# Performance work log

Measured on AMD Instinct MI355X. Metric: run time of the kernel, lower is better.

The kernel has to match this reference:

```python
import jax, jax.numpy as jnp
import numpy as np
from jax import lax

B, T, L = 16, 200, 250
IDIM, ODIM, DUNITS = 512, 80, 1024
ATT_DIM, ACONV_CHANS, ACONV_K = 128, 32, 31
PRENET = 256


def setup_inputs() -> dict:
    key = jax.random.key(0)
    ks = iter(jax.random.split(key, 40))
    def nrm(shape, fan_in):
        return jax.random.normal(next(ks), shape, jnp.float32) * (fan_in ** -0.5)
    inp = {}
    inp['hs'] = jax.random.normal(next(ks), (B, T, IDIM), jnp.float32)
    inp['hlens'] = jax.random.randint(next(ks), (B,), T // 2, T + 1)
    inp['ys'] = jax.random.normal(next(ks), (B, L, ODIM), jnp.float32)
    # location-aware attention params
    inp['W_enc'] = nrm((IDIM, ATT_DIM), IDIM)
    inp['b_enc'] = jnp.zeros((ATT_DIM,), jnp.float32)
    inp['W_dec'] = nrm((DUNITS, ATT_DIM), DUNITS)
    inp['W_att'] = nrm((ACONV_CHANS, ATT_DIM), ACONV_CHANS)
    inp['loc_conv_w'] = nrm((ACONV_CHANS, 1, ACONV_K), ACONV_K)
    inp['gvec_w'] = nrm((ATT_DIM,), ATT_DIM)
    inp['gvec_b'] = jnp.zeros((), jnp.float32)
    # prenet (no bias, dropout off in eval)
    inp['prenet_W1'] = nrm((ODIM, PRENET), ODIM)
    inp['prenet_W2'] = nrm((PRENET, PRENET), PRENET)
    # LSTM cells (torch gate order i,f,g,o; bih+bhh folded into one bias)
    in0 = IDIM + PRENET
    inp['Wih0'] = nrm((4 * DUNITS, in0), in0)
    inp['Whh0'] = nrm((4 * DUNITS, DUNITS), DUNITS)
    inp['b0'] = jnp.zeros((4 * DUNITS,), jnp.float32)
    inp['Wih1'] = nrm((4 * DUNITS, DUNITS), DUNITS)
    inp['Whh1'] = nrm((4 * DUNITS, DUNITS), DUNITS)
    inp['b1'] = jnp.zeros((4 * DUNITS,), jnp.float32)
    # output heads
    inp['feat_W'] = nrm((DUNITS, ODIM), DUNITS)
    inp['prob_W'] = nrm((DUNITS,), DUNITS)
    inp['prob_b'] = jnp.zeros((), jnp.float32)
    # postnet: conv(no bias) + BN(eval; running mean=0, var=1 folded away) + tanh
    inp['post_w_in'] = nrm((512, ODIM, 5), 5 * ODIM)
    inp['post_g_in'] = jnp.ones((512,), jnp.float32)
    inp['post_b_in'] = jnp.zeros((512,), jnp.float32)
    inp['post_w_mid'] = nrm((3, 512, 512, 5), 5 * 512)
    inp['post_g_mid'] = jnp.ones((3, 512), jnp.float32)
    inp['post_b_mid'] = jnp.zeros((3, 512), jnp.float32)
    inp['post_w_out'] = nrm((ODIM, 512, 5), 5 * 512)
    inp['post_g_out'] = jnp.ones((ODIM,), jnp.float32)
    inp['post_b_out'] = jnp.zeros((ODIM,), jnp.float32)
    return inp


def _conv1d(x, w, pad):
    # x: [B, Cin, T], w: [Cout, Cin, K]
    return lax.conv_general_dilated(x, w, (1,), [(pad, pad)],
                                    dimension_numbers=('NCH', 'OIH', 'NCH'))


def _lstm(x, h, c, Wih, Whh, b):
    g = x @ Wih.T + h @ Whh.T + b
    i, f, gg, o = jnp.split(g, 4, axis=-1)
    c2 = jax.nn.sigmoid(f) * c + jax.nn.sigmoid(i) * jnp.tanh(gg)
    return jax.nn.sigmoid(o) * jnp.tanh(c2), c2


def reference(hs, hlens, ys, W_enc, b_enc, W_dec, W_att, loc_conv_w, gvec_w, gvec_b,
              prenet_W1, prenet_W2, Wih0, Whh0, b0, Wih1, Whh1, b1,
              feat_W, prob_W, prob_b,
              post_w_in, post_g_in, post_b_in, post_w_mid, post_g_mid, post_b_mid,
              post_w_out, post_g_out, post_b_out):
    mask = jnp.arange(T)[None, :] < hlens[:, None]            # [B,T]
    pre_enc = hs @ W_enc + b_enc                              # [B,T,A] precomputed
    # teacher forcing: prenet input at step i is ys[:, i-1] (zeros at i=0);
    # prenet has no recurrent dependency -> vectorize over time
    prev = jnp.concatenate([jnp.zeros((B, 1, ODIM), hs.dtype), ys[:, :L - 1]], axis=1)
    pren = jax.nn.relu(jax.nn.relu(prev @ prenet_W1) @ prenet_W2)  # [B,L,256]
    att_w0 = mask.astype(hs.dtype) / hlens[:, None].astype(hs.dtype)
    z = jnp.zeros((B, DUNITS), hs.dtype)
    carry0 = (z, z, z, z, att_w0)

    def step(carry, pren_t):
        z0, c0, z1, c1, att_w = carry
        conv = _conv1d(att_w[:, None, :], loc_conv_w, ACONV_K // 2)   # [B,C,T]
        e = jnp.tanh(pre_enc + jnp.einsum('bct,ca->bta', conv, W_att)
                     + (z0 @ W_dec)[:, None, :]) @ gvec_w + gvec_b    # [B,T]
        e = jnp.where(mask, e, -1e30)
        w = jax.nn.softmax(2.0 * e, axis=1)                           # scaling=2.0
        att_c = jnp.einsum('bt,btd->bd', w, hs)
        x = jnp.concatenate([att_c, pren_t], axis=1)
        z0n, c0n = _lstm(x, z0, c0, Wih0, Whh0, b0)
        z1n, c1n = _lstm(z0n, z1, c1, Wih1, Whh1, b1)
        return (z0n, c0n, z1n, c1n, w), (z1n @ feat_W, z1n @ prob_W + prob_b)

    _, (outs, probs) = lax.scan(step, carry0, jnp.swapaxes(pren, 0, 1))
    outs = jnp.transpose(outs, (1, 2, 0))   # [B, odim, L] (matches torch.stack dim=2)
    probs = probs.T                         # [B, L]
    # postnet (BN in eval with running mean=0/var=1 reduces to gamma*x+beta)
    h = jnp.tanh(post_g_in[:, None] * _conv1d(outs, post_w_in, 2) + post_b_in[:, None])
    for i in range(3):
        h = jnp.tanh(post_g_mid[i][:, None] * _conv1d(h, post_w_mid[i], 2)
                     + post_b_mid[i][:, None])
    h = post_g_out[:, None] * _conv1d(h, post_w_out, 2) + post_b_out[:, None]
    post_outs = outs + h
    return jnp.swapaxes(post_outs, 1, 2), jnp.swapaxes(outs, 1, 2), probs
```

## Files before the change

### kernel.cpp

```cpp
#include <hip/hip_runtime.h>
#include <cstdint>
#include <cstddef>

constexpr int B_ = 16, T_ = 200, L_ = 250;
constexpr int IDIM = 512, ODIM = 80, DUNITS = 1024;
constexpr int ADIM = 128, ACH = 32, AK = 31;
constexpr int PRE = 256;
constexpr int TPAD = 208;

typedef _Float16 h16;
typedef _Float16 half8 __attribute__((ext_vector_type(8)));
typedef _Float16 half4 __attribute__((ext_vector_type(4)));
typedef float f32x4 __attribute__((ext_vector_type(4)));

constexpr int FSTEP = 352;
constexpr int FZ0W = 0, FZ0AGG = 256, FDPW = 288, FAW = 320;

constexpr size_t OFF_PE    = 0;
constexpr size_t OFF_H0H   = 851968;
constexpr size_t OFF_Z1H   = 917504;
constexpr size_t OFF_ATTC  = 983040;
constexpr size_t OFF_DP    = 999424;
constexpr size_t OFF_FLAGS = 1007616;
constexpr size_t ZERO_BYTES= 1359616;
constexpr size_t OFF_MB    = 1359616;
constexpr size_t OFF_WDR   = 1367808;
constexpr size_t OFF_PREN  = 1629952;
constexpr size_t OFF_HSH   = 3677952;
constexpr size_t OFF_W0AH  = 6954752;
constexpr size_t OFF_WHH0  = 13246208;
constexpr size_t OFF_WI1   = 21634816;
constexpr size_t OFF_WHH1  = 30023424;
constexpr size_t OFF_Z1ALL = 38412032;
constexpr size_t OFF_OUTS  = 54796032;
constexpr size_t OFF_PA    = 56076032;
constexpr size_t OFF_PB    = 64268032;

__device__ __forceinline__ float fsig(float x) {
  x = fminf(fmaxf(x, -30.f), 30.f);
  return __builtin_amdgcn_rcpf(1.f + __expf(-x));
}
__device__ __forceinline__ float ftanh(float x) {
  x = fminf(fmaxf(x, -15.f), 15.f);
  const float e = __expf(2.f * x);
  return (e - 1.f) * __builtin_amdgcn_rcpf(e + 1.f);
}
__device__ __forceinline__ f32x4 mfma16(half8 a, half8 b, f32x4 c) {
  return __builtin_amdgcn_mfma_f32_16x16x32_f16(a, b, c, 0, 0, 0);
}
__device__ __forceinline__ half8 load8_agent(const h16* p) {
  union { unsigned long long q[2]; half8 v; } cv;
  cv.q[0] = __hip_atomic_load((const unsigned long long*)p, __ATOMIC_RELAXED,
                              __HIP_MEMORY_SCOPE_AGENT);
  cv.q[1] = __hip_atomic_load(((const unsigned long long*)p) + 1, __ATOMIC_RELAXED,
                              __HIP_MEMORY_SCOPE_AGENT);
  return cv.v;
}
__device__ __forceinline__ float loadf_agent(const float* p) {
  union { unsigned u; float f; } cv;
  cv.u = __hip_atomic_load((const unsigned*)p, __ATOMIC_RELAXED,
                           __HIP_MEMORY_SCOPE_AGENT);
  return cv.f;
}
__device__ __forceinline__ void storef_agent(float* p, float v) {
  union { unsigned u; float f; } cv; cv.f = v;
  __hip_atomic_store((unsigned*)p, cv.u, __ATOMIC_RELAXED, __HIP_MEMORY_SCOPE_AGENT);
}
__device__ __forceinline__ int loadw(const int* p) {
  return __hip_atomic_load(p, __ATOMIC_RELAXED, __HIP_MEMORY_SCOPE_AGENT);
}
__device__ __forceinline__ void storew(int* p, int v) {
  __hip_atomic_store(p, v, __ATOMIC_RELAXED, __HIP_MEMORY_SCOPE_AGENT);
}
__device__ __forceinline__ void poll_n(const int* base, const int n) {
  if ((int)threadIdx.x < n) {
    const int* f = base + threadIdx.x;
    while (loadw(f) == 0) __builtin_amdgcn_s_sleep(1);
  }
  __syncthreads();
  __builtin_amdgcn_sched_barrier(0);
}
__device__ __forceinline__ void poll_all256(const int* base) {
  const int* f = base + threadIdx.x;
  while (loadw(f) == 0) __builtin_amdgcn_s_sleep(1);
  __syncthreads();
  __builtin_amdgcn_sched_barrier(0);
}
__device__ __forceinline__ void flag_set(int* w) {
  asm volatile("s_waitcnt vmcnt(0)" ::: "memory");
  __syncthreads();
  if (threadIdx.x == 0) storew(w, 1);
}


__global__ void k_zero(float4* __restrict__ p, int n4) {
  const int i = blockIdx.x * blockDim.x + threadIdx.x;
  if (i < n4) p[i] = make_float4(0.f, 0.f, 0.f, 0.f);
}

__global__ void __launch_bounds__(128) k_preenc(const float* __restrict__ hs,
    const float* __restrict__ W_enc, const float* __restrict__ b_enc,
    h16* __restrict__ pe_h) {
  const int bt = blockIdx.x, b = bt / T_, tt = bt % T_;
  __shared__ float s[IDIM];
  for (int i = threadIdx.x; i < IDIM; i += 128) s[i] = hs[(size_t)bt * IDIM + i];
  __syncthreads();
  const int a = threadIdx.x;
  float acc = b_enc[a];
#pragma unroll 4
  for (int d = 0; d < IDIM; ++d) acc += s[d] * W_enc[d * ADIM + a];
  pe_h[((size_t)b * ADIM + a) * TPAD + tt] = (h16)acc;
}

__global__ void k_precMb(const float* __restrict__ lconv, const float* __restrict__ W_att,
                         h16* __restrict__ Mb) {
  const int at = blockIdx.x, lane = threadIdx.x;
  const int a = at * 16 + (lane & 15);
  const int k0 = (lane >> 4) * 8;
  half8 o;
#pragma unroll
  for (int j = 0; j < 8; ++j) {
    const int k = k0 + j;
    float v = 0.f;
    if (k < AK)
      for (int c = 0; c < ACH; ++c) v += lconv[c * AK + k] * W_att[c * ADIM + a];
    o[j] = (h16)v;
  }
  *(half8*)(Mb + (size_t)(at * 64 + lane) * 8) = o;
}

__global__ void k_cvt_perm(const float* __restrict__ src, h16* __restrict__ dst,
                           const int K) {
  const int rr = blockIdx.x;
  const int u = rr >> 2, g = rr & 3;
  const float* s = src + (size_t)(g * 1024 + u) * K;
  h16* d = dst + (size_t)rr * K;
  for (int k = threadIdx.x; k < K; k += 256) d[k] = (h16)s[k];
}

__global__ void k_cvt_wdec(const float* __restrict__ Wdec, h16* __restrict__ Wdr) {
  const int a = blockIdx.x;
  for (int k = threadIdx.x; k < 1024; k += 256)
    Wdr[(size_t)a * 1024 + k] = (h16)Wdec[(size_t)k * ADIM + a];
}

__global__ void k_cvt_f32f16(const float* __restrict__ src, h16* __restrict__ dst) {
  const size_t i = ((size_t)blockIdx.x * 256 + threadIdx.x) * 4;
  const float4 v = *(const float4*)(src + i);
  half4 o; o[0] = (h16)v.x; o[1] = (h16)v.y; o[2] = (h16)v.z; o[3] = (h16)v.w;
  *(half4*)(dst + i) = o;
}

__global__ void k_prenet1(const float* __restrict__ ys, const float* __restrict__ W1,
                          float* __restrict__ h1) {
  const int bl = blockIdx.x, b = bl / L_, l = bl % L_;
  __shared__ float s[ODIM];
  if (threadIdx.x < ODIM)
    s[threadIdx.x] = (l == 0) ? 0.f : ys[((size_t)b * L_ + l - 1) * ODIM + threadIdx.x];
  __syncthreads();
  const int p = threadIdx.x;
  float acc = 0.f;
#pragma unroll 4
  for (int o = 0; o < ODIM; ++o) acc += s[o] * W1[o * PRE + p];
  h1[(size_t)bl * PRE + p] = fmaxf(acc, 0.f);
}

__global__ void k_prenet2h(const float* __restrict__ h1, const float* __restrict__ W2,
                           h16* __restrict__ pren_h) {
  const int bl = blockIdx.x, b = bl / L_, ll = bl % L_;
  __shared__ float s[PRE];
  s[threadIdx.x] = h1[(size_t)bl * PRE + threadIdx.x];
  __syncthreads();
  const int p = threadIdx.x;
  float acc = 0.f;
#pragma unroll 4
  for (int o = 0; o < PRE; ++o) acc += s[o] * W2[o * PRE + p];
  pren_h[((size_t)ll * B_ + b) * PRE + p] = (h16)fmaxf(acc, 0.f);
}


struct ScanP {
  const h16 *pe_h, *Mb, *Wdr, *hs_h, *pren_h;
  const h16 *W0ah, *Whh0h, *Wz01h, *Whh1h;
  h16 *h0h, *z1h, *attc;
  float *dp;
  const float *gvw, *b0, *b1;
  const int *hlens;
  float *z1all;
  int *flags;
};

__device__ __forceinline__ void lstm0_partA(const h16* pren_t, const h16* z0_prev,
    const half8 wA[6], const half8 wH[8], f32x4& acc) {
  const int lane = threadIdx.x & 63, wave = threadIdx.x >> 6;
  const int nloc = lane & 15, kl8 = (lane >> 4) * 8;
#pragma unroll
  for (int c = 0; c < 8; ++c)
    acc = mfma16(load8_agent(z0_prev + nloc * DUNITS + wave * 256 + c * 32 + kl8),
                 wH[c], acc);
#pragma unroll
  for (int c = 0; c < 6; ++c) {
    const int kg = wave * 192 + c * 32;
    if (kg >= 512)
      acc = mfma16(*(const half8*)(pren_t + nloc * PRE + (kg - 512) + kl8), wA[c], acc);
  }
}

__device__ __forceinline__ void lstm0_partB(const ScanP& P, h16* z0_out, const int slab,
    const half8 wA[6], float& c0reg, f32x4 acc,
    float sred[4][64][5], float sg[16][20], h16* sho) {
  const int tid = threadIdx.x;
  const int lane = tid & 63, wave = tid >> 6;
  const int nloc = lane & 15, kl8 = (lane >> 4) * 8;
#pragma unroll
  for (int c = 0; c < 6; ++c) {
    const int kg = wave * 192 + c * 32;
    if (kg < 512)
      acc = mfma16(load8_agent(P.attc + nloc * IDIM + kg + kl8), wA[c], acc);
  }
#pragma unroll
  for (int r = 0; r < 4; ++r) sred[wave][lane][r] = acc[r];
  __syncthreads();
  {
    const float v = sred[0][lane][wave] + sred[1][lane][wave]
                  + sred[2][lane][wave] + sred[3][lane][wave];
    sg[lane & 15][4 * (lane >> 4) + wave] = v;
  }
  __syncthreads();
  if (tid < 64) {
    const int ul = tid >> 4, b = tid & 15;
    const int u = slab * 4 + ul;
    const float xi = sg[ul * 4 + 0][b] + P.b0[u];
    const float xf = sg[ul * 4 + 1][b] + P.b0[1024 + u];
    const float xg = sg[ul * 4 + 2][b] + P.b0[2048 + u];
    const float xo = sg[ul * 4 + 3][b] + P.b0[3072 + u];
    const float cn = fsig(xf) * c0reg + fsig(xi) * ftanh(xg);
    c0reg = cn;
    sho[ul * 16 + b] = (h16)(fsig(xo) * ftanh(cn));
  }
  __syncthreads();
  if (tid < 16) {
    union { h16 h[4]; unsigned long long q; } u4;
#pragma unroll
    for (int j = 0; j < 4; ++j) u4.h[j] = sho[j * 16 + tid];
    __hip_atomic_store((unsigned long long*)(z0_out + tid * DUNITS + slab * 4), u4.q,
                       __ATOMIC_RELAXED, __HIP_MEMORY_SCOPE_AGENT);
  }
}

__device__ __forceinline__ void do_lstm1(const ScanP& P,
    const h16* z0_prev, const h16* z1_prev, h16* z1_out, float* z1all_s,
    const int slab, const half8 wI[8], const half8 wHH[8], float& c1reg,
    float sred[4][64][5], float sg[16][20], h16* sho) {
  const int tid = threadIdx.x;
  const int lane = tid & 63, wave = tid >> 6;
  const int nloc = lane & 15, kl8 = (lane >> 4) * 8;
  f32x4 acc = {0.f, 0.f, 0.f, 0.f};
#pragma unroll
  for (int c = 0; c < 8; ++c)
    acc = mfma16(load8_agent(z0_prev + nloc * DUNITS + wave * 256 + c * 32 + kl8),
                 wI[c], acc);
#pragma unroll
  for (int c = 0; c < 8; ++c)
    acc = mfma16(load8_agent(z1_prev + nloc * DUNITS + wave * 256 + c * 32 + kl8),
                 wHH[c], acc);
#pragma unroll
  for (int r = 0; r < 4; ++r) sred[wave][lane][r] = acc[r];
  __syncthreads();
  {
    const float v = sred[0][lane][wave] + sred[1][lane][wave]
                  + sred[2][lane][wave] + sred[3][lane][wave];
    sg[lane & 15][4 * (lane >> 4) + wave] = v;
  }
  __syncthreads();
  if (tid < 64) {
    const int ul = tid >> 4, b = tid & 15;
    const int u = slab * 4 + ul;
    const float xi = sg[ul * 4 + 0][b] + P.b1[u];
    const float xf = sg[ul * 4 + 1][b] + P.b1[1024 + u];
    const float xg = sg[ul * 4 + 2][b] + P.b1[2048 + u];
    const float xo = sg[ul * 4 + 3][b] + P.b1[3072 + u];
    const float cn = fsig(xf) * c1reg + fsig(xi) * ftanh(xg);
    c1reg = cn;
    const float hn = fsig(xo) * ftanh(cn);
    z1all_s[b * DUNITS + u] = hn;
    sho[ul * 16 + b] = (h16)hn;
  }
  __syncthreads();
  if (tid < 16) {
    union { h16 h[4]; unsigned long long q; } u4;
#pragma unroll
    for (int j = 0; j < 4; ++j) u4.h[j] = sho[j * 16 + tid];
    __hip_atomic_store((unsigned long long*)(z1_out + tid * DUNITS + slab * 4), u4.q,
                       __ATOMIC_RELAXED, __HIP_MEMORY_SCOPE_AGENT);
  }
}

__global__ void __launch_bounds__(256, 1) k_scan(const ScanP P) {
  __shared__ float s_red[4][64][5];
  __shared__ float s_g[16][20];
  __shared__ h16   s_ho[64];
  __shared__ float s_aw[240];
  __shared__ float s_dp[ADIM];
  __shared__ float s_gv[ADIM];
  __shared__ float s_ew[256];
  __shared__ float s_wt[208];
  __shared__ float s_par[4][512];
  __shared__ float s_r8[8];
  __shared__ float s_bc[2];
  __shared__ float s_cvpe[13][8][64][4];

  const int blk = blockIdx.x, tid = threadIdx.x;
  const int lane = tid & 63, wave = tid >> 6;
  constexpr int BD = B_ * DUNITS;

  if (blk < 16) {
    const int b = blk;
    const int hl = P.hlens[b];
    const int mtmax = (hl + 15) >> 4;
    const int slab = 240 + b;
    const int l15 = lane & 15;
    half8 bfrag[8];
#pragma unroll
    for (int at = 0; at < 8; ++at)
      bfrag[at] = *(const half8*)(P.Mb + (size_t)(at * 64 + lane) * 8);
    half8 wA[6], wH[8];
    {
      const int nloc = lane & 15, kl8 = (lane >> 4) * 8;
      const h16* wrA = P.W0ah + ((size_t)(slab * 16 + nloc)) * 768 + wave * 192 + kl8;
      const h16* wrH = P.Whh0h + ((size_t)(slab * 16 + nloc)) * 1024 + wave * 256 + kl8;
#pragma unroll
      for (int c = 0; c < 6; ++c) wA[c] = *(const half8*)(wrA + c * 32);
#pragma unroll
      for (int c = 0; c < 8; ++c) wH[c] = *(const half8*)(wrH + c * 32);
    }
    if (tid < 240) {
      const int tt = tid - 15;
      s_aw[tid] = (tt >= 0 && tt < hl) ? (1.f / (float)hl) : 0.f;
    }
    if (tid < ADIM) s_gv[tid] = P.gvw[tid];
    __syncthreads();
    float c0reg = 0.f;

    for (int mi = 0; mi < 4; ++mi) {
      const int mt = wave + mi * 4;
      if (mt < mtmax) {
        half8 af;
#pragma unroll
        for (int j = 0; j < 8; ++j)
          af[j] = (h16)s_aw[mt * 16 + l15 + (lane >> 4) * 8 + j];
        const int t0 = mt * 16 + 4 * (lane >> 4);
#pragma unroll
        for (int at = 0; at < 8; ++at) {
          f32x4 z4 = {0.f, 0.f, 0.f, 0.f};
          const f32x4 cv = mfma16(af, bfrag[at], z4);
          const int a = at * 16 + l15;
          const half4 pe4 = *(const half4*)(P.pe_h + ((size_t)b * ADIM + a) * TPAD + t0);
          float4 o;
          o.x = cv[0] + (float)pe4[0]; o.y = cv[1] + (float)pe4[1];
          o.z = cv[2] + (float)pe4[2]; o.w = cv[3] + (float)pe4[3];
          *(float4*)&s_cvpe[mt][at][lane][0] = o;
        }
      }
    }
    __syncthreads();

    for (int i = 0; i < L_; ++i) {
      const h16* z0_prev = P.h0h + (size_t)(i & 1) * BD;
      h16* z0_out = P.h0h + (size_t)((i & 1) ^ 1) * BD;
      int* sf = P.flags + (size_t)i * FSTEP;
      poll_n(sf + FDPW, 8);
      if (tid < ADIM) s_dp[tid] = loadf_agent(P.dp + b * ADIM + tid);
      __syncthreads();
#pragma unroll
      for (int mi = 0; mi < 4; ++mi) {
        const int mt = wave + mi * 4;
        if (mt < mtmax) {
          const int t0 = mt * 16 + 4 * (lane >> 4);
          float e0 = 0.f, e1 = 0.f, e2 = 0.f, e3 = 0.f;
#pragma unroll
          for (int at = 0; at < 8; ++at) {
            const float4 v = *(const float4*)&s_cvpe[mt][at][lane][0];
            const int a = at * 16 + l15;
            const float g = s_gv[a], d = s_dp[a];
            e0 += g * ftanh(v.x + d);
            e1 += g * ftanh(v.y + d);
            e2 += g * ftanh(v.z + d);
            e3 += g * ftanh(v.w + d);
          }
#pragma unroll
          for (int o = 1; o < 16; o <<= 1) {
            e0 += __shfl_xor(e0, o); e1 += __shfl_xor(e1, o);
            e2 += __shfl_xor(e2, o); e3 += __shfl_xor(e3, o);
          }
          if (l15 == 0) {
            s_ew[t0 + 0] = e0; s_ew[t0 + 1] = e1; s_ew[t0 + 2] = e2; s_ew[t0 + 3] = e3;
          }
        }
      }
      __syncthreads();
      const float val = (tid < hl) ? 2.f * s_ew[tid] : -3.0e38f;
      float m = val;
#pragma unroll
      for (int o = 32; o > 0; o >>= 1) m = fmaxf(m, __shfl_xor(m, o));
      if ((tid & 63) == 0) s_r8[tid >> 6] = m;
      __syncthreads();
      if (tid == 0) s_bc[0] = fmaxf(fmaxf(s_r8[0], s_r8[1]), fmaxf(s_r8[2], s_r8[3]));
      __syncthreads();
      const float pp = (tid < hl) ? __expf(val - s_bc[0]) : 0.f;
      float ssum = pp;
#pragma unroll
      for (int o = 32; o > 0; o >>= 1) ssum += __shfl_xor(ssum, o);
      if ((tid & 63) == 0) s_r8[4 + (tid >> 6)] = ssum;
      __syncthreads();
      if (tid == 0) s_bc[1] = __builtin_amdgcn_rcpf(s_r8[4] + s_r8[5] + s_r8[6] + s_r8[7]);
      __syncthreads();
      if (tid < T_) {
        const float w = pp * s_bc[1];
        s_wt[tid] = w;
        s_aw[15 + tid] = w;
      }
      __syncthreads();
      const h16* hsb = P.hs_h + (size_t)b * T_ * IDIM;
      {
        const int d0 = lane * 8;
        float a8[8] = {0.f, 0.f, 0.f, 0.f, 0.f, 0.f, 0.f, 0.f};
        for (int tt = wave; tt < hl; tt += 4) {
          const float wt = s_wt[tt];
          const half8 hv = *(const half8*)(hsb + (size_t)tt * IDIM + d0);
#pragma unroll
          for (int j = 0; j < 8; ++j) a8[j] += wt * (float)hv[j];
        }
#pragma unroll
        for (int j = 0; j < 8; ++j) s_par[wave][d0 + j] = a8[j];
      }
      __syncthreads();
      {
        const int d = tid * 2;
        const float cx0 = s_par[0][d] + s_par[1][d] + s_par[2][d] + s_par[3][d];
        const float cx1 = s_par[0][d + 1] + s_par[1][d + 1] + s_par[2][d + 1]
                        + s_par[3][d + 1];
        union { h16 h[2]; unsigned u; } cv;
        cv.h[0] = (h16)cx0; cv.h[1] = (h16)cx1;
        __hip_atomic_store((unsigned*)(P.attc + b * IDIM + d), cv.u,
                           __ATOMIC_RELAXED, __HIP_MEMORY_SCOPE_AGENT);
      }
      flag_set(sf + FAW + b);
      f32x4 acc0 = {0.f, 0.f, 0.f, 0.f};
      lstm0_partA(P.pren_h + (size_t)i * (B_ * PRE), z0_prev, wA, wH, acc0);
      poll_n(sf + FAW, 16);
      lstm0_partB(P, z0_out, slab, wA, c0reg, acc0, s_red, s_g, s_ho);
      flag_set(sf + FZ0W + blk);
      for (int mi = 0; mi < 4; ++mi) {
        const int mt = wave + mi * 4;
        if (mt < mtmax) {
          half8 af;
#pragma unroll
          for (int j = 0; j < 8; ++j)
            af[j] = (h16)s_aw[mt * 16 + l15 + (lane >> 4) * 8 + j];
          const int t0 = mt * 16 + 4 * (lane >> 4);
#pragma unroll
          for (int at = 0; at < 8; ++at) {
            f32x4 z4 = {0.f, 0.f, 0.f, 0.f};
            const f32x4 cv = mfma16(af, bfrag[at], z4);
            const int a = at * 16 + l15;
            const half4 pe4 = *(const half4*)(P.pe_h + ((size_t)b * ADIM + a) * TPAD + t0);
            float4 o;
            o.x = cv[0] + (float)pe4[0]; o.y = cv[1] + (float)pe4[1];
            o.z = cv[2] + (float)pe4[2]; o.w = cv[3] + (float)pe4[3];
            *(float4*)&s_cvpe[mt][at][lane][0] = o;
          }
        }
      }
      __syncthreads();
    }
    return;
  }

  const int g = blk - 16;
  const bool dbl = (g < 16);
  const bool isdp = (g >= 16 && g < 24);
  half8 wA0[6], wH0[8], wI1a[8], wHH1a[8], wI1b[8], wHH1b[8], wD[8];
  {
    const int nloc = lane & 15, kl8 = (lane >> 4) * 8;
    const h16* wrA = P.W0ah + ((size_t)(g * 16 + nloc)) * 768 + wave * 192 + kl8;
    const h16* wrH = P.Whh0h + ((size_t)(g * 16 + nloc)) * 1024 + wave * 256 + kl8;
    const h16* wrI = P.Wz01h + ((size_t)(g * 16 + nloc)) * 1024 + wave * 256 + kl8;
    const h16* wrX = P.Whh1h + ((size_t)(g * 16 + nloc)) * 1024 + wave * 256 + kl8;
#pragma unroll
    for (int c = 0; c < 6; ++c) wA0[c] = *(const half8*)(wrA + c * 32);
#pragma unroll
    for (int c = 0; c < 8; ++c) wH0[c] = *(const half8*)(wrH + c * 32);
#pragma unroll
    for (int c = 0; c < 8; ++c) wI1a[c] = *(const half8*)(wrI + c * 32);
#pragma unroll
    for (int c = 0; c < 8; ++c) wHH1a[c] = *(const half8*)(wrX + c * 32);
    if (dbl) {
      const h16* wrI2 = P.Wz01h + ((size_t)((240 + g) * 16 + nloc)) * 1024 + wave * 256 + kl8;
      const h16* wrX2 = P.Whh1h + ((size_t)((240 + g) * 16 + nloc)) * 1024 + wave * 256 + kl8;
#pragma unroll
      for (int c = 0; c < 8; ++c) wI1b[c] = *(const half8*)(wrI2 + c * 32);
#pragma unroll
      for (int c = 0; c < 8; ++c) wHH1b[c] = *(const half8*)(wrX2 + c * 32);
    }
    if (isdp) {
      const h16* wrD = P.Wdr + ((size_t)((g - 16) * 16 + nloc)) * 1024 + wave * 256 + kl8;
#pragma unroll
      for (int c = 0; c < 8; ++c) wD[c] = *(const half8*)(wrD + c * 32);
    }
  }
  float c0reg = 0.f, c1a = 0.f, c1b = 0.f;

  for (int i = 0; i < L_; ++i) {
    const h16* z0_prev = P.h0h + (size_t)(i & 1) * BD;
    h16* z0_out = P.h0h + (size_t)((i & 1) ^ 1) * BD;
    int* sf = P.flags + (size_t)i * FSTEP;
    if (isdp) {
      if (i > 0) poll_all256(P.flags + (size_t)(i - 1) * FSTEP + FZ0W);
      if (tid == 0) storew(sf + FZ0AGG + (g - 16), 1);
      const int nloc = lane & 15, kl8 = (lane >> 4) * 8;
      f32x4 acc = {0.f, 0.f, 0.f, 0.f};
#pragma unroll
      for (int c = 0; c < 8; ++c)
        acc = mfma16(load8_agent(z0_prev + nloc * DUNITS + wave * 256 + c * 32 + kl8),
                     wD[c], acc);
#pragma unroll
      for (int r = 0; r < 4; ++r) s_red[wave][lane][r] = acc[r];
      __syncthreads();
      {
        const float v = s_red[0][lane][wave] + s_red[1][lane][wave]
                      + s_red[2][lane][wave] + s_red[3][lane][wave];
        const int row = lane & 15, batch = 4 * (lane >> 4) + wave;
        storef_agent(P.dp + batch * ADIM + (g - 16) * 16 + row, v);
      }
      flag_set(sf + FDPW + (g - 16));
    } else if (i > 0) {
      poll_n(sf + FZ0AGG + (blk & 7), 1);
    }
    if (i > 0) {
      const h16* z1_prev = P.z1h + (size_t)((i & 1) ^ 1) * BD;
      h16* z1_out = P.z1h + (size_t)(i & 1) * BD;
      float* z1s = P.z1all + (size_t)(i - 1) * BD;
      do_lstm1(P, z0_prev, z1_prev, z1_out, z1s, g, wI1a, wHH1a, c1a,
               s_red, s_g, s_ho);
      if (dbl)
        do_lstm1(P, z0_prev, z1_prev, z1_out, z1s, 240 + g, wI1b, wHH1b, c1b,
                 s_red, s_g, s_ho);
    }
    f32x4 acc0 = {0.f, 0.f, 0.f, 0.f};
    lstm0_partA(P.pren_h + (size_t)i * (B_ * PRE), z0_prev, wA0, wH0, acc0);
    poll_n(sf + FAW, 16);
    lstm0_partB(P, z0_out, g, wA0, c0reg, acc0, s_red, s_g, s_ho);
    flag_set(sf + FZ0W + blk);
  }
  poll_all256(P.flags + (size_t)(L_ - 1) * FSTEP + FZ0W);
  {
    const h16* z0_prev = P.h0h + (size_t)(L_ & 1) * BD;
    const h16* z1_prev = P.z1h + (size_t)((L_ & 1) ^ 1) * BD;
    h16* z1_out = P.z1h + (size_t)(L_ & 1) * BD;
    float* z1s = P.z1all + (size_t)(L_ - 1) * BD;
    do_lstm1(P, z0_prev, z1_prev, z1_out, z1s, g, wI1a, wHH1a, c1a,
             s_red, s_g, s_ho);
    if (dbl)
      do_lstm1(P, z0_prev, z1_prev, z1_out, z1s, 240 + g, wI1b, wHH1b, c1b,
               s_red, s_g, s_ho);
  }
}


__global__ void __launch_bounds__(128) k_heads(const float* __restrict__ z1_all,
    const float* __restrict__ feat_W, const float* __restrict__ prob_W,
    const float* __restrict__ prob_b, float* __restrict__ out1,
    float* __restrict__ probs, float* __restrict__ outs_bct) {
  const int bl = blockIdx.x, b = bl / L_, l = bl % L_;
  __shared__ float s_z[DUNITS];
  const float* z = z1_all + ((size_t)l * B_ + b) * DUNITS;
  for (int i = threadIdx.x; i < DUNITS; i += 128) s_z[i] = z[i];
  __syncthreads();
  const int co = threadIdx.x;
  if (co < ODIM) {
    float acc = 0.f;
#pragma unroll 4
    for (int d = 0; d < DUNITS; ++d) acc += s_z[d] * feat_W[d * ODIM + co];
    out1[((size_t)b * L_ + l) * ODIM + co] = acc;
    outs_bct[((size_t)b * ODIM + co) * L_ + l] = acc;
  } else if (co == 96) {
    float acc = prob_b[0];
#pragma unroll 4
    for (int d = 0; d < DUNITS; ++d) acc += s_z[d] * prob_W[d];
    probs[(size_t)b * L_ + l] = acc;
  }
}

template <bool TANH, bool FINAL>
__global__ void __launch_bounds__(256) k_conv(const float* __restrict__ x,
    const float* __restrict__ w, const float* __restrict__ gamma,
    const float* __restrict__ beta, float* __restrict__ y,
    const float* __restrict__ res, float* __restrict__ out0,
    const int Cin, const int Cout) {
  const int b = blockIdx.x;
  const int co0 = blockIdx.y * 8;
  const int tid = threadIdx.x;
  const int l = tid & 127;
  const int cg = tid >> 7;
  __shared__ float s_x[8][260];
  __shared__ float s_w[8][8][5];
  float acc[4][2] = {{0.f, 0.f}, {0.f, 0.f}, {0.f, 0.f}, {0.f, 0.f}};
  for (int ci0 = 0; ci0 < Cin; ci0 += 8) {
    __syncthreads();
    for (int i = tid; i < 8 * 260; i += 256) {
      const int ci = i / 260, col = i % 260;
      const int ll = col - 2;
      s_x[ci][col] = (ll >= 0 && ll < L_) ? x[((size_t)b * Cin + ci0 + ci) * L_ + ll] : 0.f;
    }
    for (int i = tid; i < 8 * 8 * 5; i += 256) {
      const int ci = i / 40, rem = i % 40, cl = rem / 5, k = rem % 5;
      s_w[ci][cl][k] = w[((size_t)(co0 + cl) * Cin + ci0 + ci) * 5 + k];
    }
    __syncthreads();
#pragma unroll 2
    for (int ci = 0; ci < 8; ++ci) {
      float xv0[5], xv1[5];
#pragma unroll
      for (int k = 0; k < 5; ++k) { xv0[k] = s_x[ci][l + k]; xv1[k] = s_x[ci][l + 128 + k]; }
#pragma unroll
      for (int j = 0; j < 4; ++j) {
        const int cl = cg * 4 + j;
#pragma unroll
        for (int k = 0; k < 5; ++k) {
          const float ww = s_w[ci][cl][k];
          acc[j][0] += ww * xv0[k];
          acc[j][1] += ww * xv1[k];
        }
      }
    }
  }
#pragma unroll
  for (int j = 0; j < 4; ++j) {
    const int co = co0 + cg * 4 + j;
    const float gm = gamma[co], bt = beta[co];
#pragma unroll
    for (int h = 0; h < 2; ++h) {
      const int ll = l + h * 128;
      if (ll < L_) {
        float v = gm * acc[j][h] + bt;
        if (TANH) v = ftanh(v);
        if (FINAL) out0[((size_t)b * L_ + ll) * ODIM + co] =
                       res[((size_t)b * ODIM + co) * L_ + ll] + v;
        else y[((size_t)b * Cout + co) * L_ + ll] = v;
      }
    }
  }
}


extern "C" void kernel_launch(void* const* d_in, const int* in_sizes, int n_in,
                              void* d_out, int out_size, void* d_ws, size_t ws_size,
                              hipStream_t stream) {
  const float* hs    = (const float*)d_in[0];
  const int*   hlens = (const int*)d_in[1];
  const float* ys    = (const float*)d_in[2];
  const float* W_enc = (const float*)d_in[3];
  const float* b_enc = (const float*)d_in[4];
  const float* W_dec = (const float*)d_in[5];
  const float* W_att = (const float*)d_in[6];
  const float* lconv = (const float*)d_in[7];
  const float* gvw   = (const float*)d_in[8];
  const float* pW1   = (const float*)d_in[10];
  const float* pW2   = (const float*)d_in[11];
  const float* Wih0  = (const float*)d_in[12];
  const float* Whh0  = (const float*)d_in[13];
  const float* b0    = (const float*)d_in[14];
  const float* Wih1  = (const float*)d_in[15];
  const float* Whh1  = (const float*)d_in[16];
  const float* b1    = (const float*)d_in[17];
  const float* featW = (const float*)d_in[18];
  const float* probW = (const float*)d_in[19];
  const float* probB = (const float*)d_in[20];
  const float* pwin  = (const float*)d_in[21];
  const float* pgin  = (const float*)d_in[22];
  const float* pbin  = (const float*)d_in[23];
  const float* pwmid = (const float*)d_in[24];
  const float* pgmid = (const float*)d_in[25];
  const float* pbmid = (const float*)d_in[26];
  const float* pwout = (const float*)d_in[27];
  const float* pgout = (const float*)d_in[28];
  const float* pbout = (const float*)d_in[29];

  char* ws = (char*)d_ws;
  h16*   pe_h   = (h16*)(ws + OFF_PE);
  h16*   h0h    = (h16*)(ws + OFF_H0H);
  h16*   z1h    = (h16*)(ws + OFF_Z1H);
  h16*   attc_h = (h16*)(ws + OFF_ATTC);
  float* dp     = (float*)(ws + OFF_DP);
  int*   flags  = (int*)(ws + OFF_FLAGS);
  h16*   Mb     = (h16*)(ws + OFF_MB);
  h16*   Wdr    = (h16*)(ws + OFF_WDR);
  h16*   pren_h = (h16*)(ws + OFF_PREN);
  h16*   hs_h   = (h16*)(ws + OFF_HSH);
  h16*   W0ah   = (h16*)(ws + OFF_W0AH);
  h16*   Whh0h  = (h16*)(ws + OFF_WHH0);
  h16*   Wz01h  = (h16*)(ws + OFF_WI1);
  h16*   Whh1h  = (h16*)(ws + OFF_WHH1);
  float* z1all  = (float*)(ws + OFF_Z1ALL);
  float* outsb  = (float*)(ws + OFF_OUTS);
  float* pa     = (float*)(ws + OFF_PA);
  float* pb     = (float*)(ws + OFF_PB);

  float* out0 = (float*)d_out;
  float* out1 = out0 + (size_t)B_ * L_ * ODIM;
  float* out2 = out1 + (size_t)B_ * L_ * ODIM;

  hipLaunchKernelGGL(k_zero, dim3((ZERO_BYTES / 16 + 255) / 256), dim3(256), 0, stream,
                     (float4*)ws, (int)(ZERO_BYTES / 16));
  hipLaunchKernelGGL(k_preenc, dim3(B_ * T_), dim3(128), 0, stream, hs, W_enc, b_enc, pe_h);
  hipLaunchKernelGGL(k_precMb, dim3(8), dim3(64), 0, stream, lconv, W_att, Mb);
  hipLaunchKernelGGL(k_cvt_perm, dim3(4096), dim3(256), 0, stream, Wih0, W0ah, 768);
  hipLaunchKernelGGL(k_cvt_perm, dim3(4096), dim3(256), 0, stream, Whh0, Whh0h, 1024);
  hipLaunchKernelGGL(k_cvt_perm, dim3(4096), dim3(256), 0, stream, Wih1, Wz01h, 1024);
  hipLaunchKernelGGL(k_cvt_perm, dim3(4096), dim3(256), 0, stream, Whh1, Whh1h, 1024);
  hipLaunchKernelGGL(k_cvt_wdec, dim3(128), dim3(256), 0, stream, W_dec, Wdr);
  hipLaunchKernelGGL(k_cvt_f32f16, dim3(1600), dim3(256), 0, stream, hs, hs_h);
  hipLaunchKernelGGL(k_prenet1, dim3(B_ * L_), dim3(PRE), 0, stream, ys, pW1, pa);
  hipLaunchKernelGGL(k_prenet2h, dim3(B_ * L_), dim3(PRE), 0, stream, pa, pW2, pren_h);

  ScanP S{pe_h, Mb, Wdr, hs_h, pren_h, W0ah, Whh0h, Wz01h, Whh1h,
          h0h, z1h, attc_h, dp, gvw, b0, b1, hlens, z1all, flags};
  hipLaunchKernelGGL(k_scan, dim3(256), dim3(256), 0, stream, S);

  hipLaunchKernelGGL(k_heads, dim3(B_ * L_), dim3(128), 0, stream,
                     z1all, featW, probW, probB, out1, out2, outsb);

  hipLaunchKernelGGL((k_conv<true, false>), dim3(B_, 64), dim3(256), 0, stream,
                     outsb, pwin, pgin, pbin, pa, nullptr, nullptr, ODIM, 512);
  hipLaunchKernelGGL((k_conv<true, false>), dim3(B_, 64), dim3(256), 0, stream,
                     pa, pwmid, pgmid, pbmid, pb, nullptr, nullptr, 512, 512);
  hipLaunchKernelGGL((k_conv<true, false>), dim3(B_, 64), dim3(256), 0, stream,
                     pb, pwmid + (size_t)512 * 512 * 5, pgmid + 512, pbmid + 512,
                     pa, nullptr, nullptr, 512, 512);
  hipLaunchKernelGGL((k_conv<true, false>), dim3(B_, 64), dim3(256), 0, stream,
                     pa, pwmid + (size_t)2 * 512 * 512 * 5, pgmid + 1024, pbmid + 1024,
                     pb, nullptr, nullptr, 512, 512);
  hipLaunchKernelGGL((k_conv<false, true>), dim3(B_, 10), dim3(256), 0, stream,
                     pb, pwout, pgout, pbout, nullptr, outsb, out0, 512, ODIM);
}
```

Baseline: 7.209 ms.

## Replicate recurrent state buffers and flags 8x to spread cross-block polling contention

The persistent scan kernel now writes its LSTM hidden states (z0, z1) and the attention context into 8 replicas, so that groups of blocks read disjoint copies. Flags are also spread across separate 32-int-strided slots per replica group, and single-thread polling replaces multi-thread polling where only one flag is needed. The aim is to cut contention on the same L2/cache lines during the per-step global synchronisation and state reads. In addition, the lstm1 input loads are issued all at once before the MFMAs, and z1all is stored in fp16 instead of fp32. In exchange, each step performs 8x as many small atomic stores, the workspace grows, and z1 precision for the output heads drops.

```diff
diff --git a/kernel.cpp b/kernel.cpp
--- a/kernel.cpp
+++ b/kernel.cpp
@@ -7,34 +7,36 @@
 constexpr int ADIM = 128, ACH = 32, AK = 31;
 constexpr int PRE = 256;
 constexpr int TPAD = 208;
+constexpr int NREP = 8;
+constexpr int BDR = 16 * 1024;
 
 typedef _Float16 h16;
 typedef _Float16 half8 __attribute__((ext_vector_type(8)));
 typedef _Float16 half4 __attribute__((ext_vector_type(4)));
 typedef float f32x4 __attribute__((ext_vector_type(4)));
 
-constexpr int FSTEP = 352;
-constexpr int FZ0W = 0, FZ0AGG = 256, FDPW = 288, FAW = 320;
+constexpr int FSTEP = 1056;
+constexpr int FZ0W = 0, FZ0AGG = 256, FDPW = 512, FAW = 544;
 
 constexpr size_t OFF_PE    = 0;
 constexpr size_t OFF_H0H   = 851968;
-constexpr size_t OFF_Z1H   = 917504;
-constexpr size_t OFF_ATTC  = 983040;
-constexpr size_t OFF_DP    = 999424;
-constexpr size_t OFF_FLAGS = 1007616;
-constexpr size_t ZERO_BYTES= 1359616;
-constexpr size_t OFF_MB    = 1359616;
-constexpr size_t OFF_WDR   = 1367808;
-constexpr size_t OFF_PREN  = 1629952;
-constexpr size_t OFF_HSH   = 3677952;
-constexpr size_t OFF_W0AH  = 6954752;
-constexpr size_t OFF_WHH0  = 13246208;
-constexpr size_t OFF_WI1   = 21634816;
-constexpr size_t OFF_WHH1  = 30023424;
-constexpr size_t OFF_Z1ALL = 38412032;
-constexpr size_t OFF_OUTS  = 54796032;
-constexpr size_t OFF_PA    = 56076032;
-constexpr size_t OFF_PB    = 64268032;
+constexpr size_t OFF_Z1H   = 1376256;
+constexpr size_t OFF_ATTC  = 1900544;
+constexpr size_t OFF_DP    = 2031616;
+constexpr size_t OFF_FLAGS = 2039808;
+constexpr size_t ZERO_BYTES= 3095808;
+constexpr size_t OFF_MB    = 3095808;
+constexpr size_t OFF_WDR   = 3104000;
+constexpr size_t OFF_PREN  = 3366144;
+constexpr size_t OFF_HSH   = 5414144;
+constexpr size_t OFF_W0AH  = 8690944;
+constexpr size_t OFF_WHH0  = 14982400;
+constexpr size_t OFF_WI1   = 23371008;
+constexpr size_t OFF_WHH1  = 31759616;
+constexpr size_t OFF_Z1ALL = 40148224;
+constexpr size_t OFF_OUTS  = 48340224;
+constexpr size_t OFF_PA    = 49620224;
+constexpr size_t OFF_PB    = 57812224;
 
 __device__ __forceinline__ float fsig(float x) {
   x = fminf(fmaxf(x, -30.f), 30.f);
@@ -80,16 +82,18 @@
   __syncthreads();
   __builtin_amdgcn_sched_barrier(0);
 }
+__device__ __forceinline__ void poll_one(const int* f) {
+  if (threadIdx.x == 0) {
+    while (loadw(f) == 0) __builtin_amdgcn_s_sleep(1);
+  }
+  __syncthreads();
+  __builtin_amdgcn_sched_barrier(0);
+}
 __device__ __forceinline__ void poll_all256(const int* base) {
   const int* f = base + threadIdx.x;
   while (loadw(f) == 0) __builtin_amdgcn_s_sleep(1);
   __syncthreads();
   __builtin_amdgcn_sched_barrier(0);
-}
-__device__ __forceinline__ void flag_set(int* w) {
-  asm volatile("s_waitcnt vmcnt(0)" ::: "memory");
-  __syncthreads();
-  if (threadIdx.x == 0) storew(w, 1);
 }
 
 
@@ -186,17 +190,17 @@
   float *dp;
   const float *gvw, *b0, *b1;
   const int *hlens;
-  float *z1all;
+  h16 *z1all;
   int *flags;
 };
 
-__device__ __forceinline__ void lstm0_partA(const h16* pren_t, const h16* z0_prev,
+__device__ __forceinline__ void lstm0_partA(const h16* pren_t, const h16* z0p,
     const half8 wA[6], const half8 wH[8], f32x4& acc) {
   const int lane = threadIdx.x & 63, wave = threadIdx.x >> 6;
   const int nloc = lane & 15, kl8 = (lane >> 4) * 8;
 #pragma unroll
   for (int c = 0; c < 8; ++c)
-    acc = mfma16(load8_agent(z0_prev + nloc * DUNITS + wave * 256 + c * 32 + kl8),
+    acc = mfma16(load8_agent(z0p + nloc * DUNITS + wave * 256 + c * 32 + kl8),
                  wH[c], acc);
 #pragma unroll
   for (int c = 0; c < 6; ++c) {
@@ -206,8 +210,8 @@
   }
 }
 
-__device__ __forceinline__ void lstm0_partB(const ScanP& P, h16* z0_out, const int slab,
-    const half8 wA[6], float& c0reg, f32x4 acc,
+__device__ __forceinline__ void lstm0_partB(const ScanP& P, const h16* attc_r,
+    h16* z0o, const int slab, const half8 wA[6], float& c0reg, f32x4 acc,
     float sred[4][64][5], float sg[16][20], h16* sho) {
   const int tid = threadIdx.x;
   const int lane = tid & 63, wave = tid >> 6;
@@ -216,7 +220,7 @@
   for (int c = 0; c < 6; ++c) {
     const int kg = wave * 192 + c * 32;
     if (kg < 512)
-      acc = mfma16(load8_agent(P.attc + nloc * IDIM + kg + kl8), wA[c], acc);
+      acc = mfma16(load8_agent(attc_r + nloc * IDIM + kg + kl8), wA[c], acc);
   }
 #pragma unroll
   for (int r = 0; r < 4; ++r) sred[wave][lane][r] = acc[r];
@@ -239,31 +243,27 @@
     sho[ul * 16 + b] = (h16)(fsig(xo) * ftanh(cn));
   }
   __syncthreads();
-  if (tid < 16) {
+  if (tid < 16 * NREP) {
+    const int rb = tid >> 4, bb = tid & 15;
     union { h16 h[4]; unsigned long long q; } u4;
 #pragma unroll
-    for (int j = 0; j < 4; ++j) u4.h[j] = sho[j * 16 + tid];
-    __hip_atomic_store((unsigned long long*)(z0_out + tid * DUNITS + slab * 4), u4.q,
-                       __ATOMIC_RELAXED, __HIP_MEMORY_SCOPE_AGENT);
-  }
-}
-
-__device__ __forceinline__ void do_lstm1(const ScanP& P,
-    const h16* z0_prev, const h16* z1_prev, h16* z1_out, float* z1all_s,
-    const int slab, const half8 wI[8], const half8 wHH[8], float& c1reg,
+    for (int j = 0; j < 4; ++j) u4.h[j] = sho[j * 16 + bb];
+    __hip_atomic_store((unsigned long long*)(z0o + (size_t)rb * BDR + bb * DUNITS + slab * 4),
+                       u4.q, __ATOMIC_RELAXED, __HIP_MEMORY_SCOPE_AGENT);
+  }
+}
+
+__device__ __forceinline__ void lstm1_mm(const ScanP& P, const half8 r0[8],
+    const half8 r1[8], h16* z1o, h16* z1all_s, const int slab,
+    const half8 wI[8], const half8 wHH[8], float& c1reg,
     float sred[4][64][5], float sg[16][20], h16* sho) {
   const int tid = threadIdx.x;
   const int lane = tid & 63, wave = tid >> 6;
-  const int nloc = lane & 15, kl8 = (lane >> 4) * 8;
   f32x4 acc = {0.f, 0.f, 0.f, 0.f};
 #pragma unroll
-  for (int c = 0; c < 8; ++c)
-    acc = mfma16(load8_agent(z0_prev + nloc * DUNITS + wave * 256 + c * 32 + kl8),
-                 wI[c], acc);
-#pragma unroll
-  for (int c = 0; c < 8; ++c)
-    acc = mfma16(load8_agent(z1_prev + nloc * DUNITS + wave * 256 + c * 32 + kl8),
-                 wHH[c], acc);
+  for (int c = 0; c < 8; ++c) acc = mfma16(r0[c], wI[c], acc);
+#pragma unroll
+  for (int c = 0; c < 8; ++c) acc = mfma16(r1[c], wHH[c], acc);
 #pragma unroll
   for (int r = 0; r < 4; ++r) sred[wave][lane][r] = acc[r];
   __syncthreads();
@@ -283,16 +283,18 @@
     const float cn = fsig(xf) * c1reg + fsig(xi) * ftanh(xg);
     c1reg = cn;
     const float hn = fsig(xo) * ftanh(cn);
-    z1all_s[b * DUNITS + u] = hn;
-    sho[ul * 16 + b] = (h16)hn;
-  }
-  __syncthreads();
-  if (tid < 16) {
+    const h16 hh = (h16)hn;
+    z1all_s[b * DUNITS + u] = hh;
+    sho[ul * 16 + b] = hh;
+  }
+  __syncthreads();
+  if (tid < 16 * NREP) {
+    const int rb = tid >> 4, bb = tid & 15;
     union { h16 h[4]; unsigned long long q; } u4;
 #pragma unroll
-    for (int j = 0; j < 4; ++j) u4.h[j] = sho[j * 16 + tid];
-    __hip_atomic_store((unsigned long long*)(z1_out + tid * DUNITS + slab * 4), u4.q,
-                       __ATOMIC_RELAXED, __HIP_MEMORY_SCOPE_AGENT);
+    for (int j = 0; j < 4; ++j) u4.h[j] = sho[j * 16 + bb];
+    __hip_atomic_store((unsigned long long*)(z1o + (size_t)rb * BDR + bb * DUNITS + slab * 4),
+                       u4.q, __ATOMIC_RELAXED, __HIP_MEMORY_SCOPE_AGENT);
   }
 }
 
@@ -312,7 +314,7 @@
 
   const int blk = blockIdx.x, tid = threadIdx.x;
   const int lane = tid & 63, wave = tid >> 6;
-  constexpr int BD = B_ * DUNITS;
+  const int rep = blk & 7;
 
   if (blk < 16) {
     const int b = blk;
@@ -366,8 +368,8 @@
     __syncthreads();
 
     for (int i = 0; i < L_; ++i) {
-      const h16* z0_prev = P.h0h + (size_t)(i & 1) * BD;
-      h16* z0_out = P.h0h + (size_t)((i & 1) ^ 1) * BD;
+      const h16* z0p = P.h0h + ((size_t)(i & 1) * NREP + rep) * BDR;
+      h16* z0o = P.h0h + ((size_t)((i & 1) ^ 1) * NREP) * BDR;
       int* sf = P.flags + (size_t)i * FSTEP;
       poll_n(sf + FDPW, 8);
       if (tid < ADIM) s_dp[tid] = loadf_agent(P.dp + b * ADIM + tid);
@@ -442,15 +444,22 @@
                         + s_par[3][d + 1];
         union { h16 h[2]; unsigned u; } cv;
         cv.h[0] = (h16)cx0; cv.h[1] = (h16)cx1;
-        __hip_atomic_store((unsigned*)(P.attc + b * IDIM + d), cv.u,
-                           __ATOMIC_RELAXED, __HIP_MEMORY_SCOPE_AGENT);
-      }
-      flag_set(sf + FAW + b);
+#pragma unroll
+        for (int r = 0; r < NREP; ++r)
+          __hip_atomic_store((unsigned*)(P.attc + ((size_t)r * 16 + b) * IDIM + d), cv.u,
+                             __ATOMIC_RELAXED, __HIP_MEMORY_SCOPE_AGENT);
+      }
+      asm volatile("s_waitcnt vmcnt(0)" ::: "memory");
+      __syncthreads();
+      if (tid < 16) storew(sf + FAW + tid * 32 + b, 1);
       f32x4 acc0 = {0.f, 0.f, 0.f, 0.f};
-      lstm0_partA(P.pren_h + (size_t)i * (B_ * PRE), z0_prev, wA, wH, acc0);
-      poll_n(sf + FAW, 16);
-      lstm0_partB(P, z0_out, slab, wA, c0reg, acc0, s_red, s_g, s_ho);
-      flag_set(sf + FZ0W + blk);
+      lstm0_partA(P.pren_h + (size_t)i * (B_ * PRE), z0p, wA, wH, acc0);
+      poll_n(sf + FAW + (blk & 15) * 32, 16);
+      lstm0_partB(P, P.attc + (size_t)rep * 16 * IDIM, z0o, slab, wA, c0reg, acc0,
+                  s_red, s_g, s_ho);
+      asm volatile("s_waitcnt vmcnt(0)" ::: "memory");
+      __syncthreads();
+      if (tid == 0) storew(sf + FZ0W + blk, 1);
       for (int mi = 0; mi < 4; ++mi) {
         const int mt = wave + mi * 4;
         if (mt < mtmax) {
@@ -510,19 +519,21 @@
     }
   }
   float c0reg = 0.f, c1a = 0.f, c1b = 0.f;
+  const int nloc = lane & 15, kl8 = (lane >> 4) * 8;
 
   for (int i = 0; i < L_; ++i) {
-    const h16* z0_prev = P.h0h + (size_t)(i & 1) * BD;
-    h16* z0_out = P.h0h + (size_t)((i & 1) ^ 1) * BD;
+    const h16* z0p = P.h0h + ((size_t)(i & 1) * NREP + rep) * BDR;
+    h16* z0o = P.h0h + ((size_t)((i & 1) ^ 1) * NREP) * BDR;
+    const h16* z1p = P.z1h + ((size_t)((i & 1) ^ 1) * NREP + rep) * BDR;
+    h16* z1o = P.z1h + ((size_t)(i & 1) * NREP) * BDR;
     int* sf = P.flags + (size_t)i * FSTEP;
     if (isdp) {
       if (i > 0) poll_all256(P.flags + (size_t)(i - 1) * FSTEP + FZ0W);
-      if (tid == 0) storew(sf + FZ0AGG + (g - 16), 1);
-      const int nloc = lane & 15, kl8 = (lane >> 4) * 8;
+      if (tid < 8) storew(sf + FZ0AGG + tid * 32 + (g - 16), 1);
       f32x4 acc = {0.f, 0.f, 0.f, 0.f};
 #pragma unroll
       for (int c = 0; c < 8; ++c)
-        acc = mfma16(load8_agent(z0_prev + nloc * DUNITS + wave * 256 + c * 32 + kl8),
+        acc = mfma16(load8_agent(z0p + nloc * DUNITS + wave * 256 + c * 32 + kl8),
                      wD[c], acc);
 #pragma unroll
       for (int r = 0; r < 4; ++r) s_red[wave][lane][r] = acc[r];
@@ -533,49 +544,62 @@
         const int row = lane & 15, batch = 4 * (lane >> 4) + wave;
         storef_agent(P.dp + batch * ADIM + (g - 16) * 16 + row, v);
       }
-      flag_set(sf + FDPW + (g - 16));
+      asm volatile("s_waitcnt vmcnt(0)" ::: "memory");
+      __syncthreads();
+      if (tid == 0) storew(sf + FDPW + (g - 16), 1);
     } else if (i > 0) {
-      poll_n(sf + FZ0AGG + (blk & 7), 1);
+      poll_one(sf + FZ0AGG + ((blk >> 3) & 7) * 32 + (blk & 7));
     }
     if (i > 0) {
-      const h16* z1_prev = P.z1h + (size_t)((i & 1) ^ 1) * BD;
-      h16* z1_out = P.z1h + (size_t)(i & 1) * BD;
-      float* z1s = P.z1all + (size_t)(i - 1) * BD;
-      do_lstm1(P, z0_prev, z1_prev, z1_out, z1s, g, wI1a, wHH1a, c1a,
-               s_red, s_g, s_ho);
+      half8 r0[8], r1[8];
+#pragma unroll
+      for (int c = 0; c < 8; ++c)
+        r0[c] = load8_agent(z0p + nloc * DUNITS + wave * 256 + c * 32 + kl8);
+#pragma unroll
+      for (int c = 0; c < 8; ++c)
+        r1[c] = load8_agent(z1p + nloc * DUNITS + wave * 256 + c * 32 + kl8);
+      h16* z1s = P.z1all + (size_t)(i - 1) * (B_ * DUNITS);
+      lstm1_mm(P, r0, r1, z1o, z1s, g, wI1a, wHH1a, c1a, s_red, s_g, s_ho);
       if (dbl)
-        do_lstm1(P, z0_prev, z1_prev, z1_out, z1s, 240 + g, wI1b, wHH1b, c1b,
-                 s_red, s_g, s_ho);
+        lstm1_mm(P, r0, r1, z1o, z1s, 240 + g, wI1b, wHH1b, c1b, s_red, s_g, s_ho);
     }
     f32x4 acc0 = {0.f, 0.f, 0.f, 0.f};
-    lstm0_partA(P.pren_h + (size_t)i * (B_ * PRE), z0_prev, wA0, wH0, acc0);
-    poll_n(sf + FAW, 16);
-    lstm0_partB(P, z0_out, g, wA0, c0reg, acc0, s_red, s_g, s_ho);
-    flag_set(sf + FZ0W + blk);
+    lstm0_partA(P.pren_h + (size_t)i * (B_ * PRE), z0p, wA0, wH0, acc0);
+    poll_n(sf + FAW + (blk & 15) * 32, 16);
+    lstm0_partB(P, P.attc + (size_t)rep * 16 * IDIM, z0o, g, wA0, c0reg, acc0,
+                s_red, s_g, s_ho);
+    asm volatile("s_waitcnt vmcnt(0)" ::: "memory");
+    __syncthreads();
+    if (tid == 0) storew(sf + FZ0W + blk, 1);
   }
   poll_all256(P.flags + (size_t)(L_ - 1) * FSTEP + FZ0W);
   {
-    const h16* z0_prev = P.h0h + (size_t)(L_ & 1) * BD;
-    const h16* z1_prev = P.z1h + (size_t)((L_ & 1) ^ 1) * BD;
-    h16* z1_out = P.z1h + (size_t)(L_ & 1) * BD;
-    float* z1s = P.z1all + (size_t)(L_ - 1) * BD;
-    do_lstm1(P, z0_prev, z1_prev, z1_out, z1s, g, wI1a, wHH1a, c1a,
-             s_red, s_g, s_ho);
+    const h16* z0p = P.h0h + ((size_t)(L_ & 1) * NREP + rep) * BDR;
+    const h16* z1p = P.z1h + ((size_t)((L_ & 1) ^ 1) * NREP + rep) * BDR;
+    h16* z1o = P.z1h + ((size_t)(L_ & 1) * NREP) * BDR;
+    h16* z1s = P.z1all + (size_t)(L_ - 1) * (B_ * DUNITS);
+    half8 r0[8], r1[8];
+#pragma unroll
+    for (int c = 0; c < 8; ++c)
+      r0[c] = load8_agent(z0p + nloc * DUNITS + wave * 256 + c * 32 + kl8);
+#pragma unroll
+    for (int c = 0; c < 8; ++c)
+      r1[c] = load8_agent(z1p + nloc * DUNITS + wave * 256 + c * 32 + kl8);
+    lstm1_mm(P, r0, r1, z1o, z1s, g, wI1a, wHH1a, c1a, s_red, s_g, s_ho);
     if (dbl)
-      do_lstm1(P, z0_prev, z1_prev, z1_out, z1s, 240 + g, wI1b, wHH1b, c1b,
-               s_red, s_g, s_ho);
-  }
-}
-
-
-__global__ void __launch_bounds__(128) k_heads(const float* __restrict__ z1_all,
+      lstm1_mm(P, r0, r1, z1o, z1s, 240 + g, wI1b, wHH1b, c1b, s_red, s_g, s_ho);
+  }
+}
+
+
+__global__ void __launch_bounds__(128) k_heads(const h16* __restrict__ z1_all,
     const float* __restrict__ feat_W, const float* __restrict__ prob_W,
     const float* __restrict__ prob_b, float* __restrict__ out1,
     float* __restrict__ probs, float* __restrict__ outs_bct) {
   const int bl = blockIdx.x, b = bl / L_, l = bl % L_;
   __shared__ float s_z[DUNITS];
-  const float* z = z1_all + ((size_t)l * B_ + b) * DUNITS;
-  for (int i = threadIdx.x; i < DUNITS; i += 128) s_z[i] = z[i];
+  const h16* z = z1_all + ((size_t)l * B_ + b) * DUNITS;
+  for (int i = threadIdx.x; i < DUNITS; i += 128) s_z[i] = (float)z[i];
   __syncthreads();
   const int co = threadIdx.x;
   if (co < ODIM) {
@@ -702,7 +726,7 @@
   h16*   Whh0h  = (h16*)(ws + OFF_WHH0);
   h16*   Wz01h  = (h16*)(ws + OFF_WI1);
   h16*   Whh1h  = (h16*)(ws + OFF_WHH1);
-  float* z1all  = (float*)(ws + OFF_Z1ALL);
+  h16*   z1all  = (h16*)(ws + OFF_Z1ALL);
   float* outsb  = (float*)(ws + OFF_OUTS);
   float* pa     = (float*)(ws + OFF_PA);
   float* pb     = (float*)(ws + OFF_PB);
```

New measurement: 7.304 ms. Within noise of the previous version (+1.3%).
